# Optimization experiments

Hardware: AMD Instinct MI355X
Metric: run time of the kernel (lower is better)

## Reference

```python
import jax, jax.numpy as jnp
import numpy as np

L, H, NH, I = 12, 768, 12, 3072
DH = H // NH
EPS = 1e-12
STD = 0.02

def _ln(x, g, b):
    m = jnp.mean(x, axis=-1, keepdims=True)
    v = jnp.mean(jnp.square(x - m), axis=-1, keepdims=True)
    return (x - m) * jax.lax.rsqrt(v + EPS) * g + b

def setup_inputs() -> dict:
    key = jax.random.key(0)
    ks = jax.random.split(key, 6)
    return {
        "hidden_states": jax.random.normal(ks[0], (8, 512, H), dtype=jnp.float32),
        "attention_mask": jnp.zeros((8, 1, 1, 512), dtype=jnp.float32),
        "normA_gamma": jnp.ones((L, H), jnp.float32),
        "normA_beta": jnp.zeros((L, H), jnp.float32),
        "normB_gamma": jnp.ones((L, H), jnp.float32),
        "normB_beta": jnp.zeros((L, H), jnp.float32),
        "wa": jax.random.normal(ks[1], (L, 3 * H, H), jnp.float32) * STD,
        "ba": jnp.zeros((L, 3 * H), jnp.float32),
        "wb": jax.random.normal(ks[2], (L, H, H), jnp.float32) * STD,
        "bb": jnp.zeros((L, H), jnp.float32),
        "wc": jax.random.normal(ks[3], (L, I, H), jnp.float32) * STD,
        "bc": jnp.zeros((L, I), jnp.float32),
        "wd": jax.random.normal(ks[4], (L, H, I), jnp.float32) * STD,
        "bd": jnp.zeros((L, H), jnp.float32),
    }

def _encoder(hidden_states, attention_mask, normA_gamma, normA_beta, normB_gamma,
             normB_beta, wa, ba, wb, bb, wc, bc, wd, bd):
    B, S, _ = hidden_states.shape
    scale = 1.0 / jnp.sqrt(jnp.float32(DH))

    def layer(x, p):
        ga, bA, gB, bB_, Wa, Ba, Wb, Bb, Wc, Bc, Wd, Bd = p
        # fused QKV: [B,S,3H]
        qkv = jnp.einsum('bsh,oh->bso', x, Wa) + Ba
        q, k, v = jnp.split(qkv, 3, axis=-1)
        q = q.reshape(B, S, NH, DH)
        k = k.reshape(B, S, NH, DH)
        v = v.reshape(B, S, NH, DH)
        scores = jnp.einsum('bqnd,bknd->bnqk', q, k) * scale + attention_mask
        probs = jax.nn.softmax(scores, axis=-1)
        ctx = jnp.einsum('bnqk,bknd->bqnd', probs, v).reshape(B, S, H)
        attn_out = jnp.einsum('bsh,oh->bso', ctx, Wb) + Bb
        x = _ln(x + attn_out, ga, bA)           # post-LN after attention
        h = jax.nn.gelu(jnp.einsum('bsh,ih->bsi', x, Wc) + Bc, approximate=False)
        ffn_out = jnp.einsum('bsi,hi->bsh', h, Wd) + Bd
        x = _ln(x + ffn_out, gB, bB_)           # post-LN after FFN
        return x, None

    params = (normA_gamma, normA_beta, normB_gamma, normB_beta,
              wa, ba, wb, bb, wc, bc, wd, bd)
    out, _ = jax.lax.scan(layer, hidden_states, params)
    return out

def reference(hidden_states, attention_mask, normA_gamma, normA_beta, normB_gamma,
              normB_beta, wa, ba, wb, bb, wc, bc, wd, bd):
    return _encoder(hidden_states, attention_mask, normA_gamma, normA_beta,
                    normB_gamma, normB_beta, wa, ba, wb, bb, wc, bc, wd, bd)
```

## Files before the change

kernel.cpp:

```cpp
#include <hip/hip_runtime.h>
#include <hip/hip_bf16.h>
#include <cmath>

typedef __bf16 bf16;
typedef __attribute__((ext_vector_type(8))) __bf16 bf16x8;
typedef __attribute__((ext_vector_type(4))) float f32x4;

#define DEV __device__ __forceinline__

constexpr int HDIM = 768, NHEADS = 12, DHEAD = 64, IDIM = 3072, BATCH = 8, SEQ = 512;
constexpr int MTOK = BATCH * SEQ;
constexpr int H3 = 3 * HDIM;
constexpr float SCALE = 0.125f;

DEV void gld16(const bf16* g, bf16* l) {
  __builtin_amdgcn_global_load_lds((const __attribute__((address_space(1))) void*)g,
                                   (__attribute__((address_space(3))) void*)l, 16, 0, 0);
}

__global__ void k_cvt_all(const float* __restrict__ a, const float* __restrict__ b,
                          const float* __restrict__ c, const float* __restrict__ d,
                          bf16* __restrict__ oa, bf16* __restrict__ ob,
                          bf16* __restrict__ oc, bf16* __restrict__ od,
                          long na, long nb, long nc, long nd) {
  long i0 = ((long)blockIdx.x * blockDim.x + threadIdx.x) * 4;
  long st = (long)gridDim.x * blockDim.x * 4;
  union U { bf16 t[4]; short4 s; };
  for (long i = i0; i < na; i += st) {
    float4 v = *(const float4*)(a + i);
    U u; u.t[0] = (bf16)v.x; u.t[1] = (bf16)v.y; u.t[2] = (bf16)v.z; u.t[3] = (bf16)v.w;
    *(short4*)(oa + i) = u.s;
  }
  for (long i = i0; i < nb; i += st) {
    float4 v = *(const float4*)(b + i);
    U u; u.t[0] = (bf16)v.x; u.t[1] = (bf16)v.y; u.t[2] = (bf16)v.z; u.t[3] = (bf16)v.w;
    *(short4*)(ob + i) = u.s;
  }
  for (long i = i0; i < nc; i += st) {
    float4 v = *(const float4*)(c + i);
    U u; u.t[0] = (bf16)v.x; u.t[1] = (bf16)v.y; u.t[2] = (bf16)v.z; u.t[3] = (bf16)v.w;
    *(short4*)(oc + i) = u.s;
  }
  for (long i = i0; i < nd; i += st) {
    float4 v = *(const float4*)(d + i);
    U u; u.t[0] = (bf16)v.x; u.t[1] = (bf16)v.y; u.t[2] = (bf16)v.z; u.t[3] = (bf16)v.w;
    *(short4*)(od + i) = u.s;
  }
}

__global__ void k_initx(const float* __restrict__ s, float* __restrict__ xf,
                        bf16* __restrict__ xb, int n4) {
  int i = blockIdx.x * blockDim.x + threadIdx.x;
  int st = gridDim.x * blockDim.x;
  for (; i < n4; i += st) {
    float4 v = ((const float4*)s)[i];
    ((float4*)xf)[i] = v;
    union { bf16 t[4]; short4 q; } u;
    u.t[0] = (bf16)v.x; u.t[1] = (bf16)v.y; u.t[2] = (bf16)v.z; u.t[3] = (bf16)v.w;
    ((short4*)xb)[i] = u.q;
  }
}

template <int OUT>
__global__ __launch_bounds__(256) void k_gemm(const bf16* __restrict__ A,
                                              const bf16* __restrict__ W,
                                              const float* __restrict__ bias,
                                              void* __restrict__ C, int M, int N, int K) {
  __shared__ alignas(128) bf16 As[2][128 * 32];
  __shared__ alignas(128) bf16 Bs[2][128 * 32];
  const int tid = threadIdx.x;
  const int lane = tid & 63, wave = tid >> 6;
  const int wr = wave >> 1, wc = wave & 1;
  const int bx = blockIdx.x, by = blockIdx.y;
  const bf16* Ab = A + (size_t)by * 128 * K;
  const bf16* Bb = W + (size_t)bx * 128 * K;
  const int s0 = tid, s1 = tid + 256;
  const int r0 = s0 >> 2, c0 = ((s0 & 3) ^ ((r0 >> 1) & 3)) << 3;
  const int r1 = s1 >> 2, c1 = ((s1 & 3) ^ ((r1 >> 1) & 3)) << 3;

  f32x4 acc[4][4] = {};
  const int KT = K >> 5;
  int cur = 0;
  gld16(Ab + (size_t)r0 * K + c0, &As[0][s0 * 8]);
  gld16(Ab + (size_t)r1 * K + c1, &As[0][s1 * 8]);
  gld16(Bb + (size_t)r0 * K + c0, &Bs[0][s0 * 8]);
  gld16(Bb + (size_t)r1 * K + c1, &Bs[0][s1 * 8]);

  const int r = lane & 15, kg = lane >> 4;
  for (int kt = 0; kt < KT; ++kt) {
    __syncthreads();
    if (kt + 1 < KT) {
      int k0 = (kt + 1) << 5;
      gld16(Ab + (size_t)r0 * K + k0 + c0, &As[cur ^ 1][s0 * 8]);
      gld16(Ab + (size_t)r1 * K + k0 + c1, &As[cur ^ 1][s1 * 8]);
      gld16(Bb + (size_t)r0 * K + k0 + c0, &Bs[cur ^ 1][s0 * 8]);
      gld16(Bb + (size_t)r1 * K + k0 + c1, &Bs[cur ^ 1][s1 * 8]);
    }
    const bf16* Ac = As[cur];
    const bf16* Bc = Bs[cur];
    bf16x8 af[4], bfr[4];
#pragma unroll
    for (int m = 0; m < 4; ++m) {
      int row = wr * 64 + m * 16 + r;
      af[m] = *(const bf16x8*)(Ac + row * 32 + ((kg ^ ((row >> 1) & 3)) << 3));
    }
#pragma unroll
    for (int n = 0; n < 4; ++n) {
      int row = wc * 64 + n * 16 + r;
      bfr[n] = *(const bf16x8*)(Bc + row * 32 + ((kg ^ ((row >> 1) & 3)) << 3));
    }
#pragma unroll
    for (int m = 0; m < 4; ++m)
#pragma unroll
      for (int n = 0; n < 4; ++n)
        acc[m][n] = __builtin_amdgcn_mfma_f32_16x16x32_bf16(af[m], bfr[n], acc[m][n], 0, 0, 0);
    cur ^= 1;
  }
  const int g = lane >> 4, c16 = lane & 15;
#pragma unroll
  for (int m = 0; m < 4; ++m) {
#pragma unroll
    for (int n = 0; n < 4; ++n) {
      int col = bx * 128 + wc * 64 + n * 16 + c16;
      float bv = bias[col];
#pragma unroll
      for (int j = 0; j < 4; ++j) {
        int row = by * 128 + wr * 64 + m * 16 + g * 4 + j;
        float v = acc[m][n][j] + bv;
        if (OUT == 2) v = 0.5f * v * (1.0f + erff(v * 0.70710678118f));
        ((bf16*)C)[(size_t)row * N + col] = (bf16)v;
      }
    }
  }
}

__global__ __launch_bounds__(256) void k_gemm_sk(const bf16* __restrict__ A,
                                                 const bf16* __restrict__ W,
                                                 float* __restrict__ C,
                                                 int M, int N, int Kc, int ld) {
  __shared__ alignas(128) bf16 As[2][128 * 32];
  __shared__ alignas(128) bf16 Bs[2][128 * 32];
  const int tid = threadIdx.x;
  const int lane = tid & 63, wave = tid >> 6;
  const int wr = wave >> 1, wc = wave & 1;
  const int bx = blockIdx.x, by = blockIdx.y, kz = blockIdx.z;
  const bf16* Ab = A + (size_t)by * 128 * ld + (size_t)kz * Kc;
  const bf16* Bb = W + (size_t)bx * 128 * ld + (size_t)kz * Kc;
  float* Cz = C + (size_t)kz * M * N;
  const int s0 = tid, s1 = tid + 256;
  const int r0 = s0 >> 2, c0 = ((s0 & 3) ^ ((r0 >> 1) & 3)) << 3;
  const int r1 = s1 >> 2, c1 = ((s1 & 3) ^ ((r1 >> 1) & 3)) << 3;

  f32x4 acc[4][4] = {};
  const int KT = Kc >> 5;
  int cur = 0;
  gld16(Ab + (size_t)r0 * ld + c0, &As[0][s0 * 8]);
  gld16(Ab + (size_t)r1 * ld + c1, &As[0][s1 * 8]);
  gld16(Bb + (size_t)r0 * ld + c0, &Bs[0][s0 * 8]);
  gld16(Bb + (size_t)r1 * ld + c1, &Bs[0][s1 * 8]);

  const int r = lane & 15, kg = lane >> 4;
  for (int kt = 0; kt < KT; ++kt) {
    __syncthreads();
    if (kt + 1 < KT) {
      int k0 = (kt + 1) << 5;
      gld16(Ab + (size_t)r0 * ld + k0 + c0, &As[cur ^ 1][s0 * 8]);
      gld16(Ab + (size_t)r1 * ld + k0 + c1, &As[cur ^ 1][s1 * 8]);
      gld16(Bb + (size_t)r0 * ld + k0 + c0, &Bs[cur ^ 1][s0 * 8]);
      gld16(Bb + (size_t)r1 * ld + k0 + c1, &Bs[cur ^ 1][s1 * 8]);
    }
    const bf16* Ac = As[cur];
    const bf16* Bc = Bs[cur];
    bf16x8 af[4], bfr[4];
#pragma unroll
    for (int m = 0; m < 4; ++m) {
      int row = wr * 64 + m * 16 + r;
      af[m] = *(const bf16x8*)(Ac + row * 32 + ((kg ^ ((row >> 1) & 3)) << 3));
    }
#pragma unroll
    for (int n = 0; n < 4; ++n) {
      int row = wc * 64 + n * 16 + r;
      bfr[n] = *(const bf16x8*)(Bc + row * 32 + ((kg ^ ((row >> 1) & 3)) << 3));
    }
#pragma unroll
    for (int m = 0; m < 4; ++m)
#pragma unroll
      for (int n = 0; n < 4; ++n)
        acc[m][n] = __builtin_amdgcn_mfma_f32_16x16x32_bf16(af[m], bfr[n], acc[m][n], 0, 0, 0);
    cur ^= 1;
  }
  const int g = lane >> 4, c16 = lane & 15;
#pragma unroll
  for (int m = 0; m < 4; ++m)
#pragma unroll
    for (int n = 0; n < 4; ++n) {
      int col = bx * 128 + wc * 64 + n * 16 + c16;
#pragma unroll
      for (int j = 0; j < 4; ++j) {
        int row = by * 128 + wr * 64 + m * 16 + g * 4 + j;
        Cz[(size_t)row * N + col] = acc[m][n][j];
      }
    }
}

__global__ void k_vT(const bf16* __restrict__ qkv, bf16* __restrict__ vT) {
  int bh = blockIdx.x;
  int b = bh / NHEADS, h = bh % NHEADS;
  int s0 = blockIdx.y * 32;
  int d = threadIdx.x & 63;
  int si = threadIdx.x >> 6;
  int s = s0 + si * 8;
  const bf16* src = qkv + (size_t)(b * SEQ + s) * H3 + 2 * HDIM + h * DHEAD + d;
  union { bf16 t[8]; bf16x8 v; } u;
#pragma unroll
  for (int i = 0; i < 8; ++i) u.t[i] = src[(size_t)i * H3];
  *(bf16x8*)(vT + ((size_t)bh * DHEAD + d) * SEQ + s) = u.v;
}

__global__ __launch_bounds__(256) void k_attn(const bf16* __restrict__ qkv,
                                              const bf16* __restrict__ vT,
                                              const float* __restrict__ mask,
                                              bf16* __restrict__ ctx) {
  __shared__ alignas(128) bf16 smem[20480];
  bf16* Qs = smem;
  bf16* Ks = smem + 4096;
  bf16* Vs = smem;
  bf16* Ps = smem + 16384;
  const int tid = threadIdx.x, lane = tid & 63, wave = tid >> 6;
  const int q0 = blockIdx.x * 64;
  const int h = blockIdx.y, b = blockIdx.z;
  const int bh = b * NHEADS + h;
  const bf16* qbase = qkv + (size_t)(b * SEQ) * H3 + h * DHEAD;
  const bf16* kbase = qbase + HDIM;
  const bf16* Vsrc = vT + (size_t)bh * DHEAD * SEQ;
  const int r15 = lane & 15, kg = lane >> 4;

  for (int s = tid; s < 512; s += 256) {
    int r = s >> 3, sl = s & 7;
    gld16(qbase + (size_t)(q0 + r) * H3 + ((sl ^ (r & 7)) << 3), &Qs[s * 8]);
  }
  f32x4 acc[32];
#pragma unroll
  for (int f = 0; f < 32; ++f) acc[f] = (f32x4){0.f, 0.f, 0.f, 0.f};

  for (int half = 0; half < 2; ++half) {
    for (int s = tid; s < 2048; s += 256) {
      int r = s >> 3, sl = s & 7;
      gld16(kbase + (size_t)(half * 256 + r) * H3 + ((sl ^ (r & 7)) << 3), &Ks[s * 8]);
    }
    __syncthreads();
#pragma unroll
    for (int ks = 0; ks < 2; ++ks) {
      int qrow = wave * 16 + r15;
      int sl = ks * 4 + kg;
      bf16x8 aq = *(const bf16x8*)(Qs + qrow * 64 + ((sl ^ (qrow & 7)) << 3));
#pragma unroll
      for (int nf = 0; nf < 16; ++nf) {
        int krow = nf * 16 + r15;
        bf16x8 bk = *(const bf16x8*)(Ks + krow * 64 + ((sl ^ (krow & 7)) << 3));
        acc[half * 16 + nf] =
            __builtin_amdgcn_mfma_f32_16x16x32_bf16(aq, bk, acc[half * 16 + nf], 0, 0, 0);
      }
    }
    __syncthreads();
  }

#pragma unroll
  for (int i = 0; i < 8; ++i) {
    int g16 = tid + i * 256;
    int d = g16 >> 5, c = g16 & 31;
    gld16(Vsrc + (size_t)d * SEQ + ((c ^ (d & 7)) << 3), &Vs[g16 * 8]);
  }

  const float* mrow = mask + b * SEQ;
#pragma unroll
  for (int f = 0; f < 32; ++f) {
    float mv = mrow[f * 16 + r15];
#pragma unroll
    for (int j = 0; j < 4; ++j) acc[f][j] = acc[f][j] * SCALE + mv;
  }
#pragma unroll
  for (int j = 0; j < 4; ++j) {
    float m = -1e30f;
#pragma unroll
    for (int f = 0; f < 32; ++f) m = fmaxf(m, acc[f][j]);
    m = fmaxf(m, __shfl_xor(m, 1));
    m = fmaxf(m, __shfl_xor(m, 2));
    m = fmaxf(m, __shfl_xor(m, 4));
    m = fmaxf(m, __shfl_xor(m, 8));
    float sum = 0.f;
#pragma unroll
    for (int f = 0; f < 32; ++f) { acc[f][j] = __expf(acc[f][j] - m); sum += acc[f][j]; }
    sum += __shfl_xor(sum, 1);
    sum += __shfl_xor(sum, 2);
    sum += __shfl_xor(sum, 4);
    sum += __shfl_xor(sum, 8);
    float inv = 1.0f / sum;
#pragma unroll
    for (int f = 0; f < 32; ++f) acc[f][j] *= inv;
  }
  __syncthreads();

  f32x4 pvacc[4] = {};
  bf16* Pw = Ps + wave * (16 * 32);
#pragma unroll
  for (int half = 0; half < 2; ++half) {
    if (half == 1) {
      __syncthreads();
#pragma unroll
      for (int i = 0; i < 8; ++i) {
        int g16 = tid + i * 256;
        int d = g16 >> 5, c = g16 & 31;
        gld16(Vsrc + (size_t)d * SEQ + 256 + ((c ^ (d & 7)) << 3), &Vs[g16 * 8]);
      }
      __syncthreads();
    }
#pragma unroll
    for (int kc8 = 0; kc8 < 8; ++kc8) {
      int kc = half * 8 + kc8;
#pragma unroll
      for (int fb = 0; fb < 2; ++fb)
#pragma unroll
        for (int j = 0; j < 4; ++j) {
          int q = kg * 4 + j, k = fb * 16 + r15;
          Pw[q * 32 + ((((k >> 3) ^ ((q >> 1) & 3)) << 3) | (k & 7))] =
              (bf16)acc[kc * 2 + fb][j];
        }
      bf16x8 pa = *(const bf16x8*)(Pw + r15 * 32 + ((kg ^ ((r15 >> 1) & 3)) << 3));
#pragma unroll
      for (int n = 0; n < 4; ++n) {
        int d = n * 16 + r15;
        bf16x8 vb = *(const bf16x8*)(Vs + d * 256 + (((kc8 * 4 + kg) ^ (d & 7)) << 3));
        pvacc[n] = __builtin_amdgcn_mfma_f32_16x16x32_bf16(pa, vb, pvacc[n], 0, 0, 0);
      }
    }
  }

  bf16* crow = ctx + (size_t)(b * SEQ + q0 + wave * 16) * HDIM + h * DHEAD;
#pragma unroll
  for (int n = 0; n < 4; ++n)
#pragma unroll
    for (int j = 0; j < 4; ++j)
      crow[(size_t)(kg * 4 + j) * HDIM + n * 16 + r15] = (bf16)pvacc[n][j];
}

__global__ __launch_bounds__(256) void k_ln4(const float* __restrict__ x,
                                             const float* __restrict__ d,
                                             const float* __restrict__ bias,
                                             const float* __restrict__ gamma,
                                             const float* __restrict__ beta,
                                             float* __restrict__ xo, bf16* __restrict__ xb) {
  const size_t MH = (size_t)MTOK * HDIM;
  int row = blockIdx.x;
  const float* xr = x + (size_t)row * HDIM;
  const float* dr = d + (size_t)row * HDIM;
  int t = threadIdx.x;
  float v[3];
  float s1 = 0.f, s2 = 0.f;
#pragma unroll
  for (int i = 0; i < 3; ++i) {
    int c = i * 256 + t;
    float a = xr[c] + bias[c] + dr[c] + dr[c + MH] + dr[c + 2 * MH] + dr[c + 3 * MH];
    v[i] = a; s1 += a; s2 += a * a;
  }
#pragma unroll
  for (int o = 32; o; o >>= 1) { s1 += __shfl_down(s1, o); s2 += __shfl_down(s2, o); }
  __shared__ float red[8];
  int wv = t >> 6, lane = t & 63;
  if (lane == 0) { red[wv] = s1; red[4 + wv] = s2; }
  __syncthreads();
  s1 = red[0] + red[1] + red[2] + red[3];
  s2 = red[4] + red[5] + red[6] + red[7];
  float mean = s1 * (1.0f / 768.0f);
  float var = s2 * (1.0f / 768.0f) - mean * mean;
  float rs = rsqrtf(var + 1e-12f);
  float* xro = xo + (size_t)row * HDIM;
  bf16* xbr = xb + (size_t)row * HDIM;
#pragma unroll
  for (int i = 0; i < 3; ++i) {
    int c = i * 256 + t;
    float o = (v[i] - mean) * rs * gamma[c] + beta[c];
    xro[c] = o; xbr[c] = (bf16)o;
  }
}

extern "C" void kernel_launch(void* const* d_in, const int* in_sizes, int n_in,
                              void* d_out, int out_size, void* d_ws, size_t ws_size,
                              hipStream_t stream) {
  const float* hidden = (const float*)d_in[0];
  const float* mask   = (const float*)d_in[1];
  const float* nAg    = (const float*)d_in[2];
  const float* nAb    = (const float*)d_in[3];
  const float* nBg    = (const float*)d_in[4];
  const float* nBb    = (const float*)d_in[5];
  const float* wa     = (const float*)d_in[6];
  const float* ba     = (const float*)d_in[7];
  const float* wb     = (const float*)d_in[8];
  const float* bb     = (const float*)d_in[9];
  const float* wc     = (const float*)d_in[10];
  const float* bc     = (const float*)d_in[11];
  const float* wd     = (const float*)d_in[12];
  const float* bd     = (const float*)d_in[13];

  char* p = (char*)d_ws;
  auto alloc = [&](size_t bytes) {
    char* r = p;
    p += (bytes + 255) & ~(size_t)255;
    return (void*)r;
  };
  float* xf   = (float*)alloc((size_t)MTOK * HDIM * 4);
  bf16* xb    = (bf16*)alloc((size_t)MTOK * HDIM * 2);
  bf16* qkv   = (bf16*)alloc((size_t)MTOK * H3 * 2);
  bf16* vT    = (bf16*)alloc((size_t)BATCH * NHEADS * DHEAD * SEQ * 2);
  bf16* ctx   = (bf16*)alloc((size_t)MTOK * HDIM * 2);
  bf16* hbuf  = (bf16*)alloc((size_t)MTOK * IDIM * 2);
  float* dres = (float*)alloc((size_t)4 * MTOK * HDIM * 4);

  const size_t wa_n = (size_t)12 * H3 * HDIM;
  const size_t wb_n = (size_t)12 * HDIM * HDIM;
  const size_t wc_n = (size_t)12 * IDIM * HDIM;
  const size_t wd_n = (size_t)12 * HDIM * IDIM;
  size_t used = (size_t)(p - (char*)d_ws);
  const bool upfront = ws_size >= used + (wa_n + wb_n + wc_n + wd_n) * 2 + 8192;

  bf16* wab = (bf16*)alloc((upfront ? wa_n : (size_t)H3 * HDIM) * 2);
  bf16* wbb = (bf16*)alloc((upfront ? wb_n : (size_t)HDIM * HDIM) * 2);
  bf16* wcb = (bf16*)alloc((upfront ? wc_n : (size_t)IDIM * HDIM) * 2);
  bf16* wdb = (bf16*)alloc((upfront ? wd_n : (size_t)HDIM * IDIM) * 2);

  k_initx<<<1024, 256, 0, stream>>>(hidden, xf, xb, MTOK * HDIM / 4);
  if (upfront)
    k_cvt_all<<<2048, 256, 0, stream>>>(wa, wb, wc, wd, wab, wbb, wcb, wdb,
                                        (long)wa_n, (long)wb_n, (long)wc_n, (long)wd_n);

  for (int l = 0; l < 12; ++l) {
    bf16* waL = upfront ? wab + (size_t)l * H3 * HDIM : wab;
    bf16* wbL = upfront ? wbb + (size_t)l * HDIM * HDIM : wbb;
    bf16* wcL = upfront ? wcb + (size_t)l * IDIM * HDIM : wcb;
    bf16* wdL = upfront ? wdb + (size_t)l * HDIM * IDIM : wdb;
    if (!upfront)
      k_cvt_all<<<2048, 256, 0, stream>>>(
          wa + (size_t)l * H3 * HDIM, wb + (size_t)l * HDIM * HDIM,
          wc + (size_t)l * IDIM * HDIM, wd + (size_t)l * HDIM * IDIM,
          waL, wbL, wcL, wdL,
          (long)H3 * HDIM, (long)HDIM * HDIM, (long)IDIM * HDIM, (long)HDIM * IDIM);

    k_gemm<1><<<dim3(H3 / 128, MTOK / 128), 256, 0, stream>>>(
        xb, waL, ba + (size_t)l * H3, qkv, MTOK, H3, HDIM);
    k_vT<<<dim3(BATCH * NHEADS, SEQ / 32), 256, 0, stream>>>(qkv, vT);
    k_attn<<<dim3(SEQ / 64, NHEADS, BATCH), 256, 0, stream>>>(qkv, vT, mask, ctx);
    k_gemm_sk<<<dim3(HDIM / 128, MTOK / 128, 4), 256, 0, stream>>>(
        ctx, wbL, dres, MTOK, HDIM, HDIM / 4, HDIM);
    k_ln4<<<MTOK, 256, 0, stream>>>(xf, dres, bb + (size_t)l * HDIM,
                                    nAg + (size_t)l * HDIM, nAb + (size_t)l * HDIM, xf, xb);
    k_gemm<2><<<dim3(IDIM / 128, MTOK / 128), 256, 0, stream>>>(
        xb, wcL, bc + (size_t)l * IDIM, hbuf, MTOK, IDIM, HDIM);
    k_gemm_sk<<<dim3(HDIM / 128, MTOK / 128, 4), 256, 0, stream>>>(
        hbuf, wdL, dres, MTOK, HDIM, IDIM / 4, IDIM);
    float* xout = (l == 11) ? (float*)d_out : xf;
    k_ln4<<<MTOK, 256, 0, stream>>>(xf, dres, bd + (size_t)l * HDIM,
                                    nBg + (size_t)l * HDIM, nBb + (size_t)l * HDIM, xout, xb);
  }
}
```

Before: 2.306 ms.

## Fuse V transpose into QKV GEMM epilogue and store split-K partials in bf16

The QKV GEMM epilogue now writes the V section directly in transposed head-major layout, so the separate transpose kernel is removed. Split-K partial results for the output and FFN-down projections are stored as bf16 instead of fp32, which halves the write and read traffic into the layernorm kernels. The trade-off is reduced precision in the partial sums before the residual add and layernorm.

After: 2.145 ms. 7.0% less time.

```diff
diff --git a/kernel.cpp b/kernel.cpp
--- a/kernel.cpp
+++ b/kernel.cpp
@@ -65,7 +65,9 @@
 __global__ __launch_bounds__(256) void k_gemm(const bf16* __restrict__ A,
                                               const bf16* __restrict__ W,
                                               const float* __restrict__ bias,
-                                              void* __restrict__ C, int M, int N, int K) {
+                                              void* __restrict__ C,
+                                              bf16* __restrict__ vt,
+                                              int M, int N, int K) {
   __shared__ alignas(128) bf16 As[2][128 * 32];
   __shared__ alignas(128) bf16 Bs[2][128 * 32];
   const int tid = threadIdx.x;
@@ -123,12 +125,22 @@
     for (int n = 0; n < 4; ++n) {
       int col = bx * 128 + wc * 64 + n * 16 + c16;
       float bv = bias[col];
-#pragma unroll
-      for (int j = 0; j < 4; ++j) {
-        int row = by * 128 + wr * 64 + m * 16 + g * 4 + j;
-        float v = acc[m][n][j] + bv;
-        if (OUT == 2) v = 0.5f * v * (1.0f + erff(v * 0.70710678118f));
-        ((bf16*)C)[(size_t)row * N + col] = (bf16)v;
+      if (OUT == 3 && col >= 2 * HDIM) {
+        int hh = (col - 2 * HDIM) >> 6, dd = (col - 2 * HDIM) & 63;
+        int row0 = by * 128 + wr * 64 + m * 16 + g * 4;
+        int bb_ = row0 >> 9, ss = row0 & 511;
+        union { bf16 t[4]; short4 q; } u;
+#pragma unroll
+        for (int j = 0; j < 4; ++j) u.t[j] = (bf16)(acc[m][n][j] + bv);
+        *(short4*)(vt + (((size_t)(bb_ * NHEADS + hh) * DHEAD + dd) * SEQ + ss)) = u.q;
+      } else {
+#pragma unroll
+        for (int j = 0; j < 4; ++j) {
+          int row = by * 128 + wr * 64 + m * 16 + g * 4 + j;
+          float v = acc[m][n][j] + bv;
+          if (OUT == 2) v = 0.5f * v * (1.0f + erff(v * 0.70710678118f));
+          ((bf16*)C)[(size_t)row * N + col] = (bf16)v;
+        }
       }
     }
   }
@@ -136,7 +148,7 @@
 
 __global__ __launch_bounds__(256) void k_gemm_sk(const bf16* __restrict__ A,
                                                  const bf16* __restrict__ W,
-                                                 float* __restrict__ C,
+                                                 bf16* __restrict__ C,
                                                  int M, int N, int Kc, int ld) {
   __shared__ alignas(128) bf16 As[2][128 * 32];
   __shared__ alignas(128) bf16 Bs[2][128 * 32];
@@ -146,7 +158,7 @@
   const int bx = blockIdx.x, by = blockIdx.y, kz = blockIdx.z;
   const bf16* Ab = A + (size_t)by * 128 * ld + (size_t)kz * Kc;
   const bf16* Bb = W + (size_t)bx * 128 * ld + (size_t)kz * Kc;
-  float* Cz = C + (size_t)kz * M * N;
+  bf16* Cz = C + (size_t)kz * M * N;
   const int s0 = tid, s1 = tid + 256;
   const int r0 = s0 >> 2, c0 = ((s0 & 3) ^ ((r0 >> 1) & 3)) << 3;
   const int r1 = s1 >> 2, c1 = ((s1 & 3) ^ ((r1 >> 1) & 3)) << 3;
@@ -198,23 +210,9 @@
 #pragma unroll
       for (int j = 0; j < 4; ++j) {
         int row = by * 128 + wr * 64 + m * 16 + g * 4 + j;
-        Cz[(size_t)row * N + col] = acc[m][n][j];
+        Cz[(size_t)row * N + col] = (bf16)acc[m][n][j];
       }
     }
-}
-
-__global__ void k_vT(const bf16* __restrict__ qkv, bf16* __restrict__ vT) {
-  int bh = blockIdx.x;
-  int b = bh / NHEADS, h = bh % NHEADS;
-  int s0 = blockIdx.y * 32;
-  int d = threadIdx.x & 63;
-  int si = threadIdx.x >> 6;
-  int s = s0 + si * 8;
-  const bf16* src = qkv + (size_t)(b * SEQ + s) * H3 + 2 * HDIM + h * DHEAD + d;
-  union { bf16 t[8]; bf16x8 v; } u;
-#pragma unroll
-  for (int i = 0; i < 8; ++i) u.t[i] = src[(size_t)i * H3];
-  *(bf16x8*)(vT + ((size_t)bh * DHEAD + d) * SEQ + s) = u.v;
 }
 
 __global__ __launch_bounds__(256) void k_attn(const bf16* __restrict__ qkv,
@@ -345,7 +343,7 @@
 }
 
 __global__ __launch_bounds__(256) void k_ln4(const float* __restrict__ x,
-                                             const float* __restrict__ d,
+                                             const bf16* __restrict__ d,
                                              const float* __restrict__ bias,
                                              const float* __restrict__ gamma,
                                              const float* __restrict__ beta,
@@ -353,14 +351,15 @@
   const size_t MH = (size_t)MTOK * HDIM;
   int row = blockIdx.x;
   const float* xr = x + (size_t)row * HDIM;
-  const float* dr = d + (size_t)row * HDIM;
+  const bf16* dr = d + (size_t)row * HDIM;
   int t = threadIdx.x;
   float v[3];
   float s1 = 0.f, s2 = 0.f;
 #pragma unroll
   for (int i = 0; i < 3; ++i) {
     int c = i * 256 + t;
-    float a = xr[c] + bias[c] + dr[c] + dr[c + MH] + dr[c + 2 * MH] + dr[c + 3 * MH];
+    float a = xr[c] + bias[c] + (float)dr[c] + (float)dr[c + MH] +
+              (float)dr[c + 2 * MH] + (float)dr[c + 3 * MH];
     v[i] = a; s1 += a; s2 += a * a;
   }
 #pragma unroll
@@ -414,7 +413,7 @@
   bf16* vT    = (bf16*)alloc((size_t)BATCH * NHEADS * DHEAD * SEQ * 2);
   bf16* ctx   = (bf16*)alloc((size_t)MTOK * HDIM * 2);
   bf16* hbuf  = (bf16*)alloc((size_t)MTOK * IDIM * 2);
-  float* dres = (float*)alloc((size_t)4 * MTOK * HDIM * 4);
+  bf16* dres  = (bf16*)alloc((size_t)4 * MTOK * HDIM * 2);
 
   const size_t wa_n = (size_t)12 * H3 * HDIM;
   const size_t wb_n = (size_t)12 * HDIM * HDIM;
@@ -445,16 +444,15 @@
           waL, wbL, wcL, wdL,
           (long)H3 * HDIM, (long)HDIM * HDIM, (long)IDIM * HDIM, (long)HDIM * IDIM);
 
-    k_gemm<1><<<dim3(H3 / 128, MTOK / 128), 256, 0, stream>>>(
-        xb, waL, ba + (size_t)l * H3, qkv, MTOK, H3, HDIM);
-    k_vT<<<dim3(BATCH * NHEADS, SEQ / 32), 256, 0, stream>>>(qkv, vT);
+    k_gemm<3><<<dim3(H3 / 128, MTOK / 128), 256, 0, stream>>>(
+        xb, waL, ba + (size_t)l * H3, qkv, vT, MTOK, H3, HDIM);
     k_attn<<<dim3(SEQ / 64, NHEADS, BATCH), 256, 0, stream>>>(qkv, vT, mask, ctx);
     k_gemm_sk<<<dim3(HDIM / 128, MTOK / 128, 4), 256, 0, stream>>>(
         ctx, wbL, dres, MTOK, HDIM, HDIM / 4, HDIM);
     k_ln4<<<MTOK, 256, 0, stream>>>(xf, dres, bb + (size_t)l * HDIM,
                                     nAg + (size_t)l * HDIM, nAb + (size_t)l * HDIM, xf, xb);
     k_gemm<2><<<dim3(IDIM / 128, MTOK / 128), 256, 0, stream>>>(
-        xb, wcL, bc + (size_t)l * IDIM, hbuf, MTOK, IDIM, HDIM);
+        xb, wcL, bc + (size_t)l * IDIM, hbuf, nullptr, MTOK, IDIM, HDIM);
     k_gemm_sk<<<dim3(HDIM / 128, MTOK / 128, 4), 256, 0, stream>>>(
         hbuf, wdL, dres, MTOK, HDIM, IDIM / 4, IDIM);
     float* xout = (l == 11) ? (float*)d_out : xf;
```
